# Kernel tuning notes

Hardware: AMD Instinct MI355X
Metric: run time of the kernel (lower is better)

## Reference

```python
import jax, jax.numpy as jnp
import numpy as np

B, N, D = 8, 1024, 768
H, Z = 12, 64          # num_heads, head_dim (D = H*Z)
HID = 3072             # int(D * mlp_ratio)


def setup_inputs() -> dict:
    key = jax.random.key(0)
    k1, k2, k3, k4 = jax.random.split(key, 4)
    s = 0.02
    x = jax.random.normal(k1, (B, N, D), dtype=jnp.float32)
    Wq = jax.random.normal(k2, (D, D), dtype=jnp.float32) * s
    Wk = jax.random.normal(k3, (D, D), dtype=jnp.float32) * s
    betas = jnp.full((H,), Z ** -0.5, dtype=jnp.float32)
    W_mlp = jax.random.normal(k4, (HID, D), dtype=jnp.float32) * s
    return {"x": x, "Wq": Wq, "Wk": Wk, "betas": betas, "W_mlp": W_mlp}


def reference(x, Wq, Wk, betas, W_mlp):
    # --- KQ-aligned attention ---
    # torch Linear: y = x @ W.T ; weight shape [out=D, in=D]
    Q = jnp.einsum('bnd,ed->bne', x, Wq).reshape(B, N, H, Z).transpose(0, 2, 1, 3)  # bhqz
    K = jnp.einsum('bnd,ed->bne', x, Wk).reshape(B, N, H, Z).transpose(0, 2, 1, 3)  # bhkz
    Wq_r = Wq.reshape(H, Z, D)
    Wk_r = Wk.reshape(H, Z, D)
    F1 = jnp.einsum('hzd,bhkz->bkhd', Wq_r, K)
    F2 = jnp.einsum('hzd,bhqz->bqhd', Wk_r, Q)
    scores = jnp.einsum('bhqz,bhkz,h->bhqk', Q, K, betas)
    attn = jax.nn.softmax(scores, axis=-1)
    T1 = jnp.einsum('bkhd,bhqk->bqd', F1, attn)
    T2 = jnp.einsum('bqhd,bhqk->bkd', F2, attn)
    # --- symmetric-weight Hopfield MLP (bias=False) ---
    hid = jax.nn.relu(jnp.einsum('bnd,hd->bnh', x, W_mlp))
    mlp = jnp.einsum('bnh,hd->bnd', hid, W_mlp)
    return T1 + T2 + mlp
```

## Files before the change

### kernel.cpp

```cpp
#include <hip/hip_runtime.h>
#include <hip/hip_bf16.h>

#define Bq 8
#define Nq 1024
#define Dq 768
#define Hq 12
#define Zq 64
#define HIDq 3072
#define BN (Bq*Nq)
#define QKP 1536

typedef unsigned short u16;
typedef short s16x8 __attribute__((ext_vector_type(8)));
typedef float f32x4 __attribute__((ext_vector_type(4)));
typedef unsigned short u16x4 __attribute__((ext_vector_type(4)));

#define MFMA16 __builtin_amdgcn_mfma_f32_16x16x32_bf16
#define GLOAD16(g, l) __builtin_amdgcn_global_load_lds( \
    (const __attribute__((address_space(1))) void*)(const void*)(g), \
    (__attribute__((address_space(3))) void*)(l), 16, 0, 0)

__device__ __forceinline__ u16 f2bf(float f) {
  unsigned u = __float_as_uint(f);
  return (u16)((u + 0x7FFFu + ((u >> 16) & 1u)) >> 16);
}

__device__ __forceinline__ unsigned pk2bf(float a, float b) {
  union { __hip_bfloat162 h; unsigned u; } cv;
  cv.h.x = __float2bfloat16(a);
  cv.h.y = __float2bfloat16(b);
  return cv.u;
}

__device__ __forceinline__ void xcd_swizzle(int gx, int gy, int& bx, int& by) {
  int l = blockIdx.y * gx + blockIdx.x;
  int c = l & 7, j = l >> 3;
  by = c * (gy >> 3) + j / gx;
  bx = j % gx;
}

__global__ __launch_bounds__(256) void cvt_bf16(const float* __restrict__ in,
                                                u16* __restrict__ out, int n) {
  int i = (blockIdx.x * 256 + threadIdx.x) * 4;
  if (i >= n) return;
  float4 v = *(const float4*)&in[i];
  u16x4 o; o[0] = f2bf(v.x); o[1] = f2bf(v.y); o[2] = f2bf(v.z); o[3] = f2bf(v.w);
  *(u16x4*)&out[i] = o;
}

__global__ __launch_bounds__(256) void cvt_tr(const float* __restrict__ in,
                                              u16* __restrict__ out, u16* __restrict__ outT,
                                              int C, int out_p, int outT_p) {
  __shared__ u16 T[64][72];
  const int t = threadIdx.x;
  const int r0 = blockIdx.y * 64, c0 = blockIdx.x * 64;
  const int r = t >> 3, c8 = (t & 7) * 8;
#pragma unroll
  for (int p = 0; p < 2; p++) {
    const float* ip = &in[(size_t)(r0 + r + p * 32) * C + c0 + c8];
    float4 v0 = *(const float4*)ip, v1 = *(const float4*)(ip + 4);
    u16 tmp[8] = {f2bf(v0.x), f2bf(v0.y), f2bf(v0.z), f2bf(v0.w),
                  f2bf(v1.x), f2bf(v1.y), f2bf(v1.z), f2bf(v1.w)};
    *(uint4*)&out[(size_t)(r0 + r + p * 32) * out_p + c0 + c8] = *(uint4*)tmp;
    *(uint4*)&T[r + p * 32][c8] = *(uint4*)tmp;
  }
  __syncthreads();
#pragma unroll
  for (int p = 0; p < 2; p++) {
    int oc = r + p * 32;
    u16 tmp[8];
#pragma unroll
    for (int j = 0; j < 8; j++) tmp[j] = T[c8 + j][oc];
    *(uint4*)&outT[(size_t)(c0 + oc) * outT_p + r0 + c8] = *(uint4*)tmp;
  }
}

__global__ __launch_bounds__(256) void transpose_bf16(
    const u16* __restrict__ in, u16* __restrict__ out,
    int in_pitch, int out_pitch, int inner_n,
    long in_bs_o, long in_bs_i, long out_bs_o, long out_bs_i) {
  __shared__ u16 T[64][72];
  const int t = threadIdx.x;
  const int bz = blockIdx.z;
  const long iboff = (long)(bz / inner_n) * in_bs_o + (long)(bz % inner_n) * in_bs_i;
  const long oboff = (long)(bz / inner_n) * out_bs_o + (long)(bz % inner_n) * out_bs_i;
  const u16* ip = in + iboff + (long)(blockIdx.y * 64) * in_pitch + blockIdx.x * 64;
  u16* op = out + oboff + (long)(blockIdx.x * 64) * out_pitch + blockIdx.y * 64;
  const int r = t >> 3, c8 = (t & 7) * 8;
#pragma unroll
  for (int p = 0; p < 2; p++)
    *(uint4*)&T[r + p * 32][c8] = *(const uint4*)(ip + (size_t)(r + p * 32) * in_pitch + c8);
  __syncthreads();
#pragma unroll
  for (int p = 0; p < 2; p++) {
    int oc = r + p * 32;
    u16 tmp[8];
#pragma unroll
    for (int j = 0; j < 8; j++) tmp[j] = T[c8 + j][oc];
    *(uint4*)(op + (size_t)oc * out_pitch + c8) = *(uint4*)tmp;
  }
}

template<bool RELU>
__global__ __launch_bounds__(256) void gemm_bf16(
    const u16* __restrict__ A, const u16* __restrict__ B, u16* __restrict__ C,
    int M, int N, int K) {
  __shared__ u16 As[2][128 * 32];
  __shared__ u16 Bs[2][128 * 32];
  int bx, by;
  xcd_swizzle(gridDim.x, gridDim.y, bx, by);
  const int t = threadIdx.x, l = t & 63, w = t >> 6;
  const int lq = l & 15, quad = l >> 4;
  const int bm = by * 128, bn = bx * 128;
  const int wm = (w & 1) * 64, wn = (w >> 1) * 64;
  f32x4 acc[4][4];
#pragma unroll
  for (int i = 0; i < 4; i++)
#pragma unroll
    for (int j = 0; j < 4; j++) acc[i][j] = (f32x4){0.f, 0.f, 0.f, 0.f};

  auto stage = [&](int k0, int bufi) {
#pragma unroll
    for (int p = 0; p < 2; p++) {
      int idx = p * 256 + t;
      GLOAD16(A + (size_t)(bm + (idx >> 2)) * K + k0 + (idx & 3) * 8, &As[bufi][idx * 8]);
      GLOAD16(B + (size_t)(bn + (idx >> 2)) * K + k0 + (idx & 3) * 8, &Bs[bufi][idx * 8]);
    }
  };
  stage(0, 0);
  const int nIter = K >> 5;
  for (int it = 0; it < nIter; it++) {
    __syncthreads();
    if (it + 1 < nIter) stage((it + 1) * 32, (it + 1) & 1);
    const int bi = it & 1;
    s16x8 af[4], bf[4];
#pragma unroll
    for (int mt = 0; mt < 4; mt++)
      af[mt] = *(const s16x8*)&As[bi][(wm + mt * 16 + lq) * 32 + quad * 8];
#pragma unroll
    for (int nt = 0; nt < 4; nt++)
      bf[nt] = *(const s16x8*)&Bs[bi][(wn + nt * 16 + lq) * 32 + quad * 8];
#pragma unroll
    for (int mt = 0; mt < 4; mt++)
#pragma unroll
      for (int nt = 0; nt < 4; nt++)
        acc[mt][nt] = MFMA16(af[mt], bf[nt], acc[mt][nt], 0, 0, 0);
  }
#pragma unroll
  for (int mt = 0; mt < 4; mt++)
#pragma unroll
    for (int nt = 0; nt < 4; nt++) {
      int row = bm + wm + mt * 16 + quad * 4;
      int col = bn + wn + nt * 16 + lq;
#pragma unroll
      for (int r = 0; r < 4; r++) {
        float v = acc[mt][nt][r];
        if (RELU) v = fmaxf(v, 0.f);
        C[(size_t)(row + r) * N + col] = f2bf(v);
      }
    }
}

__global__ __launch_bounds__(256) void gemm_out2(
    const u16* __restrict__ AV12, const u16* __restrict__ hid,
    const u16* __restrict__ WqkT, const u16* __restrict__ WmT,
    float* __restrict__ out) {
  __shared__ u16 As[2][128 * 64];
  __shared__ u16 Bs[2][64 * 64];
  int bx, by;
  xcd_swizzle(gridDim.x, gridDim.y, bx, by);
  const int t = threadIdx.x, l = t & 63, w = t >> 6;
  const int lq = l & 15, quad = l >> 4;
  const int bm = by * 128, bn = bx * 64;
  const int wm = w * 32;
  f32x4 acc[2][4];
#pragma unroll
  for (int i = 0; i < 2; i++)
#pragma unroll
    for (int j = 0; j < 4; j++) acc[i][j] = (f32x4){0.f, 0.f, 0.f, 0.f};

  auto stage = [&](int tl, int bufi) {
    const u16* A; const u16* B; int pitch, k0;
    if (tl < 24) { A = AV12; B = WqkT; pitch = QKP;  k0 = tl * 64; }
    else         { A = hid;  B = WmT;  pitch = HIDq; k0 = (tl - 24) * 64; }
#pragma unroll
    for (int p = 0; p < 4; p++) {
      int idx = p * 256 + t, ks = idx >> 9, rem = idx & 511;
      GLOAD16(A + (size_t)(bm + (rem >> 2)) * pitch + k0 + ks * 32 + (rem & 3) * 8,
              &As[bufi][idx * 8]);
    }
#pragma unroll
    for (int p = 0; p < 2; p++) {
      int idx = p * 256 + t, ks = idx >> 8, rem = idx & 255;
      GLOAD16(B + (size_t)(bn + (rem >> 2)) * pitch + k0 + ks * 32 + (rem & 3) * 8,
              &Bs[bufi][idx * 8]);
    }
  };
  stage(0, 0);
  for (int tl = 0; tl < 72; tl++) {
    __syncthreads();
    if (tl + 1 < 72) stage(tl + 1, (tl + 1) & 1);
    const int bi = tl & 1;
#pragma unroll
    for (int ks = 0; ks < 2; ks++) {
      s16x8 af[2], bf[4];
#pragma unroll
      for (int mt = 0; mt < 2; mt++)
        af[mt] = *(const s16x8*)&As[bi][ks * 4096 + (wm + mt * 16 + lq) * 32 + quad * 8];
#pragma unroll
      for (int nt = 0; nt < 4; nt++)
        bf[nt] = *(const s16x8*)&Bs[bi][ks * 2048 + (nt * 16 + lq) * 32 + quad * 8];
#pragma unroll
      for (int mt = 0; mt < 2; mt++)
#pragma unroll
        for (int nt = 0; nt < 4; nt++)
          acc[mt][nt] = MFMA16(af[mt], bf[nt], acc[mt][nt], 0, 0, 0);
    }
  }
#pragma unroll
  for (int mt = 0; mt < 2; mt++)
#pragma unroll
    for (int nt = 0; nt < 4; nt++) {
      int row = bm + wm + mt * 16 + quad * 4;
      int col = bn + nt * 16 + lq;
#pragma unroll
      for (int r = 0; r < 4; r++)
        out[(size_t)(row + r) * Dq + col] = acc[mt][nt][r];
    }
}

__global__ __launch_bounds__(256) void attn_pass1(
    const u16* __restrict__ QKb, const u16* __restrict__ KbT,
    const float* __restrict__ betas, u16* __restrict__ AV12,
    float* __restrict__ lg) {
  __shared__ u16 Ps[64][72];
  __shared__ u16 Ks[2][64][32];
  __shared__ u16 Kts[2][2][64][32];

  const int t = threadIdx.x, l = t & 63, w = t >> 6;
  const int lq = l & 15, quad = l >> 4;
  const int c = blockIdx.x & 7, j = blockIdx.x >> 3;
  const int bh = c * 12 + j / 16, qt = j % 16;
  const int b = bh / Hq, h = bh % Hq;
  const int q0 = qt * 64;
  const float beta = betas[h];
  const u16* Qh = QKb + (size_t)(b * Nq) * QKP + h * 64;
  const u16* Kh = Qh + Dq;
  const u16* KTh = KbT + (size_t)bh * 64 * Nq;
  u16* QsF = &Ps[0][0];
  u16* KsF = &Ks[0][0][0];

  auto stageK = [&](int kt2) {
#pragma unroll
    for (int p = 0; p < 2; p++) {
      int idx = p * 256 + t;
      GLOAD16(Kh + (size_t)(kt2 * 64 + ((idx >> 2) & 63)) * QKP + (idx >> 8) * 32 + (idx & 3) * 8,
              KsF + idx * 8);
    }
  };
  auto stageKt = [&](int kt2, int bufi) {
#pragma unroll
    for (int p = 0; p < 2; p++) {
      int idx = p * 256 + t;
      GLOAD16(KTh + (size_t)((idx >> 2) & 63) * Nq + kt2 * 64 + (idx >> 8) * 32 + (idx & 3) * 8,
              &Kts[bufi][0][0][0] + idx * 8);
    }
  };

#pragma unroll
  for (int p = 0; p < 2; p++) {
    int idx = p * 256 + t;
    GLOAD16(Qh + (size_t)(q0 + ((idx >> 2) & 63)) * QKP + (idx >> 8) * 32 + (idx & 3) * 8,
            QsF + idx * 8);
  }
  stageK(0);
  stageKt(0, 0);
  __syncthreads();
  s16x8 bqf[2][4];
#pragma unroll
  for (int zs = 0; zs < 2; zs++)
#pragma unroll
    for (int nt = 0; nt < 4; nt++)
      bqf[zs][nt] = *(const s16x8*)&QsF[zs * 2048 + (nt * 16 + lq) * 32 + quad * 8];
  __syncthreads();

  float lsum[4] = {0.f, 0.f, 0.f, 0.f};
  f32x4 ao[4];
#pragma unroll
  for (int nt = 0; nt < 4; nt++) ao[nt] = (f32x4){0.f, 0.f, 0.f, 0.f};

  for (int kt = 0; kt < 16; kt++) {
    if (kt) __syncthreads();
    const int bi = kt & 1;
    f32x4 sc[4];
#pragma unroll
    for (int nt = 0; nt < 4; nt++) sc[nt] = (f32x4){0.f, 0.f, 0.f, 0.f};
#pragma unroll
    for (int zs = 0; zs < 2; zs++) {
      s16x8 a = *(const s16x8*)&Ks[zs][w * 16 + lq][quad * 8];
#pragma unroll
      for (int nt = 0; nt < 4; nt++)
        sc[nt] = MFMA16(a, bqf[zs][nt], sc[nt], 0, 0, 0);
    }
#pragma unroll
    for (int nt = 0; nt < 4; nt++) {
      float e0 = __expf(sc[nt][0] * beta), e1 = __expf(sc[nt][1] * beta);
      float e2 = __expf(sc[nt][2] * beta), e3 = __expf(sc[nt][3] * beta);
      lsum[nt] += (e0 + e1) + (e2 + e3);
      uint2 pk; pk.x = pk2bf(e0, e1); pk.y = pk2bf(e2, e3);
      *(uint2*)&Ps[nt * 16 + lq][w * 16 + quad * 4] = pk;
    }
    __syncthreads();
    if (kt + 1 < 16) {
      stageK(kt + 1);
      stageKt(kt + 1, (kt + 1) & 1);
    }
#pragma unroll
    for (int ks = 0; ks < 2; ks++) {
      s16x8 a = *(const s16x8*)&Ps[w * 16 + lq][ks * 32 + quad * 8];
#pragma unroll
      for (int nt = 0; nt < 4; nt++) {
        s16x8 bk = *(const s16x8*)&Kts[bi][ks][nt * 16 + lq][quad * 8];
        ao[nt] = MFMA16(a, bk, ao[nt], 0, 0, 0);
      }
    }
  }
  __syncthreads();
  float* redp = (float*)&Kts[0][0][0][0];
  float* lip  = redp + 256;
#pragma unroll
  for (int nt = 0; nt < 4; nt++) {
    float v = lsum[nt];
    v += __shfl_xor(v, 16, 64);
    v += __shfl_xor(v, 32, 64);
    if (l < 16) redp[w * 64 + nt * 16 + lq] = v;
  }
  __syncthreads();
  if (t < 64) {
    float s = redp[t] + redp[64 + t] + redp[128 + t] + redp[192 + t];
    lg[(size_t)bh * Nq + q0 + t] = s;
    lip[t] = 1.0f / s;
  }
  __syncthreads();
  u16* Oh = AV12 + (size_t)(b * Nq + q0) * QKP + h * 64;
  float lr[4];
#pragma unroll
  for (int r = 0; r < 4; r++) lr[r] = lip[w * 16 + quad * 4 + r];
#pragma unroll
  for (int nt = 0; nt < 4; nt++)
#pragma unroll
    for (int r = 0; r < 4; r++)
      Oh[(size_t)(w * 16 + quad * 4 + r) * QKP + nt * 16 + lq] = f2bf(ao[nt][r] * lr[r]);
}

__global__ __launch_bounds__(256) void attn_pass2(
    const u16* __restrict__ QKb, const u16* __restrict__ QbT,
    const float* __restrict__ betas, u16* __restrict__ AV12,
    const float* __restrict__ lg) {
  __shared__ u16 Pts[64][72];
  __shared__ u16 Qs[2][64][32];
  __shared__ u16 Qts[2][2][64][32];
  __shared__ float li_s[2][64];

  const int t = threadIdx.x, l = t & 63, w = t >> 6;
  const int lq = l & 15, quad = l >> 4;
  const int c = blockIdx.x & 7, j = blockIdx.x >> 3;
  const int bh = c * 12 + j / 16, kt = j % 16;
  const int b = bh / Hq, h = bh % Hq;
  const int k0 = kt * 64;
  const float beta = betas[h];
  const u16* Qh = QKb + (size_t)(b * Nq) * QKP + h * 64;
  const u16* Kh = Qh + Dq;
  const u16* QTh = QbT + (size_t)bh * 64 * Nq;
  u16* KsF = &Pts[0][0];
  u16* QsF = &Qs[0][0][0];

  auto stageQ = [&](int qt2) {
#pragma unroll
    for (int p = 0; p < 2; p++) {
      int idx = p * 256 + t;
      GLOAD16(Qh + (size_t)(qt2 * 64 + ((idx >> 2) & 63)) * QKP + (idx >> 8) * 32 + (idx & 3) * 8,
              QsF + idx * 8);
    }
  };
  auto stageQt = [&](int qt2, int bufi) {
#pragma unroll
    for (int p = 0; p < 2; p++) {
      int idx = p * 256 + t;
      GLOAD16(QTh + (size_t)((idx >> 2) & 63) * Nq + qt2 * 64 + (idx >> 8) * 32 + (idx & 3) * 8,
              &Qts[bufi][0][0][0] + idx * 8);
    }
  };

#pragma unroll
  for (int p = 0; p < 2; p++) {
    int idx = p * 256 + t;
    GLOAD16(Kh + (size_t)(k0 + ((idx >> 2) & 63)) * QKP + (idx >> 8) * 32 + (idx & 3) * 8,
            KsF + idx * 8);
  }
  stageQ(0);
  stageQt(0, 0);
  if (t < 64) li_s[0][t] = 1.0f / lg[(size_t)bh * Nq + t];
  __syncthreads();
  s16x8 bkf[2][4];
#pragma unroll
  for (int zs = 0; zs < 2; zs++)
#pragma unroll
    for (int nt = 0; nt < 4; nt++)
      bkf[zs][nt] = *(const s16x8*)&KsF[zs * 2048 + (nt * 16 + lq) * 32 + quad * 8];
  __syncthreads();

  f32x4 ao[4];
#pragma unroll
  for (int nt = 0; nt < 4; nt++) ao[nt] = (f32x4){0.f, 0.f, 0.f, 0.f};

  for (int qt = 0; qt < 16; qt++) {
    if (qt) __syncthreads();
    const int bi = qt & 1;
    f32x4 sc[4];
#pragma unroll
    for (int nt = 0; nt < 4; nt++) sc[nt] = (f32x4){0.f, 0.f, 0.f, 0.f};
#pragma unroll
    for (int zs = 0; zs < 2; zs++) {
      s16x8 a = *(const s16x8*)&Qs[zs][w * 16 + lq][quad * 8];
#pragma unroll
      for (int nt = 0; nt < 4; nt++)
        sc[nt] = MFMA16(a, bkf[zs][nt], sc[nt], 0, 0, 0);
    }
    float lr[4];
#pragma unroll
    for (int r = 0; r < 4; r++) lr[r] = li_s[bi][w * 16 + quad * 4 + r];
#pragma unroll
    for (int nt = 0; nt < 4; nt++) {
      float e0 = __expf(sc[nt][0] * beta) * lr[0];
      float e1 = __expf(sc[nt][1] * beta) * lr[1];
      float e2 = __expf(sc[nt][2] * beta) * lr[2];
      float e3 = __expf(sc[nt][3] * beta) * lr[3];
      uint2 pk; pk.x = pk2bf(e0, e1); pk.y = pk2bf(e2, e3);
      *(uint2*)&Pts[nt * 16 + lq][w * 16 + quad * 4] = pk;
    }
    __syncthreads();
    if (qt + 1 < 16) {
      stageQ(qt + 1);
      stageQt(qt + 1, (qt + 1) & 1);
      if (t < 64) li_s[(qt + 1) & 1][t] = 1.0f / lg[(size_t)bh * Nq + (qt + 1) * 64 + t];
    }
#pragma unroll
    for (int qs = 0; qs < 2; qs++) {
      s16x8 a = *(const s16x8*)&Pts[w * 16 + lq][qs * 32 + quad * 8];
#pragma unroll
      for (int nt = 0; nt < 4; nt++) {
        s16x8 bq = *(const s16x8*)&Qts[bi][qs][nt * 16 + lq][quad * 8];
        ao[nt] = MFMA16(a, bq, ao[nt], 0, 0, 0);
      }
    }
  }
  u16* Oh = AV12 + (size_t)(b * Nq + k0) * QKP + Dq + h * 64;
#pragma unroll
  for (int nt = 0; nt < 4; nt++)
#pragma unroll
    for (int r = 0; r < 4; r++)
      Oh[(size_t)(w * 16 + quad * 4 + r) * QKP + nt * 16 + lq] = f2bf(ao[nt][r]);
}

extern "C" void kernel_launch(void* const* d_in, const int* in_sizes, int n_in,
                              void* d_out, int out_size, void* d_ws, size_t ws_size,
                              hipStream_t stream) {
  const float* x     = (const float*)d_in[0];
  const float* Wq    = (const float*)d_in[1];
  const float* Wk    = (const float*)d_in[2];
  const float* betas = (const float*)d_in[3];
  const float* Wm    = (const float*)d_in[4];
  float* out = (float*)d_out;

  u16* xb   = (u16*)d_ws;
  u16* Wqkb = xb + (size_t)BN * Dq;
  u16* Wmb  = Wqkb + (size_t)QKP * Dq;
  u16* WqkT = Wmb + (size_t)HIDq * Dq;
  u16* QKb  = WqkT + (size_t)Dq * QKP;
  u16* QbT  = QKb + (size_t)BN * QKP;
  u16* KbT  = QbT + (size_t)Bq * Hq * Zq * Nq;
  u16* AV12 = KbT + (size_t)Bq * Hq * Zq * Nq;
  float* lg = (float*)(AV12 + (size_t)BN * QKP);
  u16* hidb = QKb;
  u16* WmT  = xb;

  dim3 blk(256);
  cvt_bf16<<<(BN * Dq) / 1024, blk, 0, stream>>>(x, xb, BN * Dq);
  cvt_tr<<<dim3(12, 12), blk, 0, stream>>>(Wq, Wqkb, WqkT, Dq, Dq, QKP);
  cvt_tr<<<dim3(12, 12), blk, 0, stream>>>(Wk, Wqkb + (size_t)Dq * Dq, WqkT + Dq, Dq, Dq, QKP);
  cvt_bf16<<<(HIDq * Dq) / 1024, blk, 0, stream>>>(Wm, Wmb, HIDq * Dq);

  gemm_bf16<false><<<dim3(QKP / 128, BN / 128), blk, 0, stream>>>(
      xb, Wqkb, QKb, BN, QKP, Dq);

  transpose_bf16<<<dim3(1, 16, 96), blk, 0, stream>>>(QKb, QbT, QKP, Nq, Hq,
      (long)Nq * QKP, 64, (long)Hq * 64 * Nq, (long)64 * Nq);
  transpose_bf16<<<dim3(1, 16, 96), blk, 0, stream>>>(QKb + Dq, KbT, QKP, Nq, Hq,
      (long)Nq * QKP, 64, (long)Hq * 64 * Nq, (long)64 * Nq);

  attn_pass1<<<Bq * Hq * 16, blk, 0, stream>>>(QKb, KbT, betas, AV12, lg);
  attn_pass2<<<Bq * Hq * 16, blk, 0, stream>>>(QKb, QbT, betas, AV12, lg);

  gemm_bf16<true><<<dim3(HIDq / 128, BN / 128), blk, 0, stream>>>(
      xb, Wmb, hidb, BN, HIDq, Dq);

  transpose_bf16<<<dim3(12, 48, 1), blk, 0, stream>>>(Wmb, WmT, Dq, HIDq, 1, 0, 0, 0, 0);

  gemm_out2<<<dim3(Dq / 64, BN / 128), blk, 0, stream>>>(AV12, hidb, WqkT, WmT, out);
}
```

Before: 359.5 us.

## Merge conversion and transpose launches and triple-buffer the output GEMM

```diff
diff --git a/kernel.cpp b/kernel.cpp
--- a/kernel.cpp
+++ b/kernel.cpp
@@ -39,29 +39,36 @@
   bx = j % gx;
 }
 
-__global__ __launch_bounds__(256) void cvt_bf16(const float* __restrict__ in,
-                                                u16* __restrict__ out, int n) {
-  int i = (blockIdx.x * 256 + threadIdx.x) * 4;
-  if (i >= n) return;
+__global__ __launch_bounds__(256) void cvt2(const float* __restrict__ x, u16* __restrict__ xb,
+                                            const float* __restrict__ Wm, u16* __restrict__ Wmb) {
+  int bid = blockIdx.x;
+  const float* in; u16* out; int i;
+  if (bid < 6144) { in = x;  out = xb;  i = bid * 1024 + threadIdx.x * 4; }
+  else            { in = Wm; out = Wmb; i = (bid - 6144) * 1024 + threadIdx.x * 4; }
   float4 v = *(const float4*)&in[i];
   u16x4 o; o[0] = f2bf(v.x); o[1] = f2bf(v.y); o[2] = f2bf(v.z); o[3] = f2bf(v.w);
   *(u16x4*)&out[i] = o;
 }
 
-__global__ __launch_bounds__(256) void cvt_tr(const float* __restrict__ in,
-                                              u16* __restrict__ out, u16* __restrict__ outT,
-                                              int C, int out_p, int outT_p) {
+__global__ __launch_bounds__(256) void cvt_tr2(const float* __restrict__ Wq,
+                                               const float* __restrict__ Wk,
+                                               u16* __restrict__ Wqkb,
+                                               u16* __restrict__ WqkT) {
   __shared__ u16 T[64][72];
   const int t = threadIdx.x;
+  const int z = blockIdx.z;
+  const float* in = z ? Wk : Wq;
+  u16* out = Wqkb + (size_t)z * Dq * Dq;
+  u16* outT = WqkT + z * Dq;
   const int r0 = blockIdx.y * 64, c0 = blockIdx.x * 64;
   const int r = t >> 3, c8 = (t & 7) * 8;
 #pragma unroll
   for (int p = 0; p < 2; p++) {
-    const float* ip = &in[(size_t)(r0 + r + p * 32) * C + c0 + c8];
+    const float* ip = &in[(size_t)(r0 + r + p * 32) * Dq + c0 + c8];
     float4 v0 = *(const float4*)ip, v1 = *(const float4*)(ip + 4);
     u16 tmp[8] = {f2bf(v0.x), f2bf(v0.y), f2bf(v0.z), f2bf(v0.w),
                   f2bf(v1.x), f2bf(v1.y), f2bf(v1.z), f2bf(v1.w)};
-    *(uint4*)&out[(size_t)(r0 + r + p * 32) * out_p + c0 + c8] = *(uint4*)tmp;
+    *(uint4*)&out[(size_t)(r0 + r + p * 32) * Dq + c0 + c8] = *(uint4*)tmp;
     *(uint4*)&T[r + p * 32][c8] = *(uint4*)tmp;
   }
   __syncthreads();
@@ -71,7 +78,7 @@
     u16 tmp[8];
 #pragma unroll
     for (int j = 0; j < 8; j++) tmp[j] = T[c8 + j][oc];
-    *(uint4*)&outT[(size_t)(c0 + oc) * outT_p + r0 + c8] = *(uint4*)tmp;
+    *(uint4*)&outT[(size_t)(c0 + oc) * QKP + r0 + c8] = *(uint4*)tmp;
   }
 }
 
@@ -98,6 +105,32 @@
 #pragma unroll
     for (int j = 0; j < 8; j++) tmp[j] = T[c8 + j][oc];
     *(uint4*)(op + (size_t)oc * out_pitch + c8) = *(uint4*)tmp;
+  }
+}
+
+__global__ __launch_bounds__(256) void head_tr(const u16* __restrict__ QKb,
+                                               u16* __restrict__ QbT,
+                                               u16* __restrict__ KbT) {
+  __shared__ u16 T[64][72];
+  const int t = threadIdx.x;
+  const int z = blockIdx.z;
+  const int half = (z >= 96) ? 1 : 0;
+  const int bhh = z - 96 * half;
+  const u16* ip = QKb + (size_t)(bhh / Hq) * Nq * QKP + (bhh % Hq) * 64 + half * Dq
+                + (size_t)(blockIdx.y * 64) * QKP;
+  u16* op = (half ? KbT : QbT) + (size_t)bhh * 64 * Nq + blockIdx.y * 64;
+  const int r = t >> 3, c8 = (t & 7) * 8;
+#pragma unroll
+  for (int p = 0; p < 2; p++)
+    *(uint4*)&T[r + p * 32][c8] = *(const uint4*)(ip + (size_t)(r + p * 32) * QKP + c8);
+  __syncthreads();
+#pragma unroll
+  for (int p = 0; p < 2; p++) {
+    int oc = r + p * 32;
+    u16 tmp[8];
+#pragma unroll
+    for (int j = 0; j < 8; j++) tmp[j] = T[c8 + j][oc];
+    *(uint4*)(op + (size_t)oc * Nq + c8) = *(uint4*)tmp;
   }
 }
 
@@ -165,8 +198,8 @@
     const u16* __restrict__ AV12, const u16* __restrict__ hid,
     const u16* __restrict__ WqkT, const u16* __restrict__ WmT,
     float* __restrict__ out) {
-  __shared__ u16 As[2][128 * 64];
-  __shared__ u16 Bs[2][64 * 64];
+  __shared__ u16 As[3][128 * 32];
+  __shared__ u16 Bs[3][64 * 32];
   int bx, by;
   xcd_swizzle(gridDim.x, gridDim.y, bx, by);
   const int t = threadIdx.x, l = t & 63, w = t >> 6;
@@ -181,41 +214,38 @@
 
   auto stage = [&](int tl, int bufi) {
     const u16* A; const u16* B; int pitch, k0;
-    if (tl < 24) { A = AV12; B = WqkT; pitch = QKP;  k0 = tl * 64; }
-    else         { A = hid;  B = WmT;  pitch = HIDq; k0 = (tl - 24) * 64; }
-#pragma unroll
-    for (int p = 0; p < 4; p++) {
-      int idx = p * 256 + t, ks = idx >> 9, rem = idx & 511;
-      GLOAD16(A + (size_t)(bm + (rem >> 2)) * pitch + k0 + ks * 32 + (rem & 3) * 8,
+    if (tl < 48) { A = AV12; B = WqkT; pitch = QKP;  k0 = tl * 32; }
+    else         { A = hid;  B = WmT;  pitch = HIDq; k0 = (tl - 48) * 32; }
+#pragma unroll
+    for (int p = 0; p < 2; p++) {
+      int idx = p * 256 + t;
+      GLOAD16(A + (size_t)(bm + (idx >> 2)) * pitch + k0 + (idx & 3) * 8,
               &As[bufi][idx * 8]);
     }
-#pragma unroll
-    for (int p = 0; p < 2; p++) {
-      int idx = p * 256 + t, ks = idx >> 8, rem = idx & 255;
-      GLOAD16(B + (size_t)(bn + (rem >> 2)) * pitch + k0 + ks * 32 + (rem & 3) * 8,
-              &Bs[bufi][idx * 8]);
-    }
+    GLOAD16(B + (size_t)(bn + (t >> 2)) * pitch + k0 + (t & 3) * 8,
+            &Bs[bufi][t * 8]);
   };
   stage(0, 0);
-  for (int tl = 0; tl < 72; tl++) {
-    __syncthreads();
-    if (tl + 1 < 72) stage(tl + 1, (tl + 1) & 1);
-    const int bi = tl & 1;
-#pragma unroll
-    for (int ks = 0; ks < 2; ks++) {
-      s16x8 af[2], bf[4];
-#pragma unroll
-      for (int mt = 0; mt < 2; mt++)
-        af[mt] = *(const s16x8*)&As[bi][ks * 4096 + (wm + mt * 16 + lq) * 32 + quad * 8];
+  stage(1, 1);
+  for (int tl = 0; tl < 144; tl++) {
+    if (tl < 143) asm volatile("s_waitcnt vmcnt(3)" ::: "memory");
+    else          asm volatile("s_waitcnt vmcnt(0)" ::: "memory");
+    __builtin_amdgcn_s_barrier();
+    __builtin_amdgcn_sched_barrier(0);
+    if (tl + 2 < 144) stage(tl + 2, (tl + 2) % 3);
+    const int bi = tl % 3;
+    s16x8 af[2], bf[4];
+#pragma unroll
+    for (int mt = 0; mt < 2; mt++)
+      af[mt] = *(const s16x8*)&As[bi][(wm + mt * 16 + lq) * 32 + quad * 8];
+#pragma unroll
+    for (int nt = 0; nt < 4; nt++)
+      bf[nt] = *(const s16x8*)&Bs[bi][(nt * 16 + lq) * 32 + quad * 8];
+#pragma unroll
+    for (int mt = 0; mt < 2; mt++)
 #pragma unroll
       for (int nt = 0; nt < 4; nt++)
-        bf[nt] = *(const s16x8*)&Bs[bi][ks * 2048 + (nt * 16 + lq) * 32 + quad * 8];
-#pragma unroll
-      for (int mt = 0; mt < 2; mt++)
-#pragma unroll
-        for (int nt = 0; nt < 4; nt++)
-          acc[mt][nt] = MFMA16(af[mt], bf[nt], acc[mt][nt], 0, 0, 0);
-    }
+        acc[mt][nt] = MFMA16(af[mt], bf[nt], acc[mt][nt], 0, 0, 0);
   }
 #pragma unroll
   for (int mt = 0; mt < 2; mt++)
@@ -486,18 +516,13 @@
   u16* WmT  = xb;
 
   dim3 blk(256);
-  cvt_bf16<<<(BN * Dq) / 1024, blk, 0, stream>>>(x, xb, BN * Dq);
-  cvt_tr<<<dim3(12, 12), blk, 0, stream>>>(Wq, Wqkb, WqkT, Dq, Dq, QKP);
-  cvt_tr<<<dim3(12, 12), blk, 0, stream>>>(Wk, Wqkb + (size_t)Dq * Dq, WqkT + Dq, Dq, Dq, QKP);
-  cvt_bf16<<<(HIDq * Dq) / 1024, blk, 0, stream>>>(Wm, Wmb, HIDq * Dq);
+  cvt2<<<8448, blk, 0, stream>>>(x, xb, Wm, Wmb);
+  cvt_tr2<<<dim3(12, 12, 2), blk, 0, stream>>>(Wq, Wk, Wqkb, WqkT);
 
   gemm_bf16<false><<<dim3(QKP / 128, BN / 128), blk, 0, stream>>>(
       xb, Wqkb, QKb, BN, QKP, Dq);
 
-  transpose_bf16<<<dim3(1, 16, 96), blk, 0, stream>>>(QKb, QbT, QKP, Nq, Hq,
-      (long)Nq * QKP, 64, (long)Hq * 64 * Nq, (long)64 * Nq);
-  transpose_bf16<<<dim3(1, 16, 96), blk, 0, stream>>>(QKb + Dq, KbT, QKP, Nq, Hq,
-      (long)Nq * QKP, 64, (long)Hq * 64 * Nq, (long)64 * Nq);
+  head_tr<<<dim3(1, 16, 192), blk, 0, stream>>>(QKb, QbT, KbT);
 
   attn_pass1<<<Bq * Hq * 16, blk, 0, stream>>>(QKb, KbT, betas, AV12, lg);
   attn_pass2<<<Bq * Hq * 16, blk, 0, stream>>>(QKb, QbT, betas, AV12, lg);
```

Result: slower. 369.9 us (+2.9%).
